# Kernel optimization log

Hardware: AMD Instinct MI355X
Metric: run time of the kernel (lower is better)

Reference implementation:

```python
import jax, jax.numpy as jnp
import numpy as np

N = 10000
E = 160000
H = 8
C = 128
D = 1024
NB = 3
NG = 64
NEG_SLOPE = 0.2
BN_EPS = 1e-5


def setup_inputs() -> dict:
    key = jax.random.key(0)
    ks = jax.random.split(key, 12)
    x = jax.random.normal(ks[0], (N, D), dtype=jnp.float32)
    edge_index = jax.random.randint(ks[1], (2, E), 0, N, dtype=jnp.int64)
    batch = jnp.sort(jax.random.randint(ks[2], (N,), 0, NG, dtype=jnp.int64))
    W = jax.random.normal(ks[3], (NB, D, D), dtype=jnp.float32) * 0.03
    att_src = jax.random.normal(ks[4], (NB, H, C), dtype=jnp.float32) * 0.1
    att_dst = jax.random.normal(ks[5], (NB, H, C), dtype=jnp.float32) * 0.1
    att_bias = jnp.zeros((NB, D), dtype=jnp.float32)
    gamma = jnp.ones((NB, D), dtype=jnp.float32)
    beta = jnp.zeros((NB, D), dtype=jnp.float32)
    W_out = jax.random.normal(ks[6], (D, 2), dtype=jnp.float32) * 0.03
    b_out = jnp.zeros((2,), dtype=jnp.float32)
    return {"x": x, "edge_index": edge_index, "batch": batch, "W": W,
            "att_src": att_src, "att_dst": att_dst, "att_bias": att_bias,
            "gamma": gamma, "beta": beta, "W_out": W_out, "b_out": b_out}


def _gat_conv(x, Wb, a_src, a_dst, bias, src, dst):
    # linear projection, per-head view: [N, H, C]
    h = (x @ Wb).reshape(N, H, C)
    alpha_src = jnp.einsum('nhc,hc->nh', h, a_src)  # [N,H]
    alpha_dst = jnp.einsum('nhc,hc->nh', h, a_dst)
    e = jax.nn.leaky_relu(alpha_src[src] + alpha_dst[dst], NEG_SLOPE)  # [Etot,H]
    # segment softmax over incoming edges per destination node
    m = jax.ops.segment_max(e, dst, num_segments=N)  # every node has self-loop
    ex = jnp.exp(e - m[dst])
    denom = jax.ops.segment_sum(ex, dst, num_segments=N)
    alpha = ex / denom[dst]  # [Etot,H]
    msg = alpha[:, :, None] * h[src]  # [Etot,H,C]
    out = jax.ops.segment_sum(msg, dst, num_segments=N).reshape(N, H * C)
    return out + bias


def _batchnorm(x, g, b):
    mu = jnp.mean(x, axis=0)
    var = jnp.mean(jnp.square(x - mu), axis=0)  # biased, training mode
    return (x - mu) * jax.lax.rsqrt(var + BN_EPS) * g + b


def reference(x, edge_index, batch, W, att_src, att_dst, att_bias, gamma, beta, W_out, b_out):
    # add self loops (PyG GATConv default)
    loop = jnp.arange(N, dtype=edge_index.dtype)
    src = jnp.concatenate([edge_index[0], loop])
    dst = jnp.concatenate([edge_index[1], loop])

    h = x
    prev = x
    for i in range(NB):
        att = _gat_conv(h, W[i], att_src[i], att_dst[i], att_bias[i], src, dst)
        o = jax.nn.relu(_batchnorm(prev + att, gamma[i], beta[i]))
        prev = h
        h = o

    # global mean pool over graphs
    sums = jax.ops.segment_sum(h, batch, num_segments=NG)
    cnts = jax.ops.segment_sum(jnp.ones((N,), dtype=h.dtype), batch, num_segments=NG)
    pooled = sums / jnp.maximum(cnts, 1.0)[:, None]
    return pooled @ W_out + b_out
```

## Files before the change

### kernel.cpp

```cpp
#include <hip/hip_runtime.h>
#include <hip/hip_bf16.h>

#define N_NODES 10000
#define E_EDGES 160000
#define ETOT    170000
#define H_HEADS 8
#define C_CH    128
#define D_DIM   1024
#define NBLK    3
#define NGRAPH  64
#define NEG_SLOPE 0.2f
#define BN_EPS  1e-5f

typedef __attribute__((ext_vector_type(8))) _Float16 half8;
typedef __attribute__((ext_vector_type(4))) _Float16 half4;
typedef __attribute__((ext_vector_type(2))) _Float16 half2v;
typedef __attribute__((ext_vector_type(4))) float f32x4;

__device__ inline int lower_bound_batch(const int* __restrict__ batch, int g) {
    int lo = 0, hi = N_NODES;
    while (lo < hi) {
        int mid = (lo + hi) >> 1;
        if (batch[mid] < g) lo = mid + 1;
        else hi = mid;
    }
    return lo;
}

__global__ void deg_kernel(const int* __restrict__ ei, int* __restrict__ deg) {
    int tid = blockIdx.x * blockDim.x + threadIdx.x;
    if (tid >= ETOT) return;
    int dst = (tid < E_EDGES) ? ei[E_EDGES + tid] : (tid - E_EDGES);
    atomicAdd(&deg[dst], 1);
}

__global__ void scan_kernel(const int* __restrict__ deg, int* __restrict__ ioff) {
    __shared__ int part[256];
    int t = threadIdx.x;
    const int CH = (N_NODES + 255) / 256;
    int base = t * CH;
    int s = 0;
    for (int j = 0; j < CH; ++j) {
        int idx = base + j;
        if (idx < N_NODES) s += deg[idx];
    }
    part[t] = s;
    __syncthreads();
    for (int o = 1; o < 256; o <<= 1) {
        int v = 0;
        if (t >= o) v = part[t - o];
        __syncthreads();
        part[t] += v;
        __syncthreads();
    }
    int run = (t == 0) ? 0 : part[t - 1];
    for (int j = 0; j < CH; ++j) {
        int idx = base + j;
        if (idx < N_NODES) { ioff[idx] = run; run += deg[idx]; }
    }
}

__global__ void scatter_kernel(const int* __restrict__ ei, int* __restrict__ ioff,
                               int* __restrict__ csr_src, int* __restrict__ csr_dst) {
    int tid = blockIdx.x * blockDim.x + threadIdx.x;
    if (tid >= ETOT) return;
    int src, dst;
    if (tid < E_EDGES) { src = ei[tid]; dst = ei[E_EDGES + tid]; }
    else { src = dst = tid - E_EDGES; }
    int pos = atomicAdd(&ioff[dst], 1);
    csr_src[pos] = src;
    csr_dst[pos] = dst;
}

__global__ __launch_bounds__(256) void xconv_kernel(const float* __restrict__ in,
                                                    _Float16* __restrict__ o, int n4) {
    int i = blockIdx.x * blockDim.x + threadIdx.x;
    if (i >= n4) return;
    float4 v = ((const float4*)in)[i];
    half4 h = {(_Float16)v.x, (_Float16)v.y, (_Float16)v.z, (_Float16)v.w};
    ((half4*)o)[i] = h;
}

__global__ __launch_bounds__(256) void wtconv_kernel(const float* __restrict__ Wall,
                                                     _Float16* __restrict__ t16all) {
    const float* W = Wall + (size_t)blockIdx.z * D_DIM * D_DIM;
    _Float16* t16 = t16all + (size_t)blockIdx.z * D_DIM * D_DIM;
    __shared__ float t[32][33];
    int bn = blockIdx.x * 32;
    int bk = blockIdx.y * 32;
    int tx = threadIdx.x & 31;
    int ty = threadIdx.x >> 5;
#pragma unroll
    for (int r = 0; r < 32; r += 8)
        t[ty + r][tx] = W[(size_t)(bk + ty + r) * D_DIM + bn + tx];
    __syncthreads();
#pragma unroll
    for (int r = 0; r < 32; r += 8)
        t16[(size_t)(bn + ty + r) * D_DIM + bk + tx] = (_Float16)t[tx][ty + r];
}

__global__ __launch_bounds__(256, 4) void gemm_mfma_kernel(const _Float16* __restrict__ A,
                                                           const _Float16* __restrict__ Bt,
                                                           _Float16* __restrict__ Hout,
                                                           const float* __restrict__ att_s,
                                                           const float* __restrict__ att_d,
                                                           float* __restrict__ asrc,
                                                           float* __restrict__ adst,
                                                           float* __restrict__ stats, int M) {
    __shared__ short As[128 * 64];
    __shared__ short Bs[64 * 64];
    int bx = blockIdx.x;
    int tid = threadIdx.x;
    if (bx == 0) {
#pragma unroll
        for (int j = 0; j < 8; ++j) stats[tid + j * 256] = 0.f;
    }
    int c = bx & 7;
    int nt = (bx >> 3) & 15;
    int mt = c + 8 * (bx >> 7);
    if (mt >= 79) return;
    int bm = mt * 128;
    int head = nt >> 1;
    int bncol = (nt & 1) * 64;
    int bnrow = nt * 64;
    int wave = tid >> 6;
    int lane = tid & 63;
    int wm = wave * 32;
    int quad = lane >> 4;
    int l16 = lane & 15;

    f32x4 acc[2][4];
#pragma unroll
    for (int i = 0; i < 2; ++i)
#pragma unroll
        for (int j = 0; j < 4; ++j) acc[i][j] = (f32x4){0.f, 0.f, 0.f, 0.f};

    int srow8 = lane >> 3;
    int sswz = ((lane & 7) ^ srow8) << 4;
    const char* gA[4];
    const char* gB[2];
    char* ldA[4];
    char* ldB[2];
#pragma unroll
    for (int r = 0; r < 4; ++r) {
        int arow = wave * 8 + r * 32 + srow8;
        int ga = bm + arow;
        if (ga > M - 1) ga = M - 1;
        gA[r] = (const char*)(A + (size_t)ga * 1024) + sswz;
        ldA[r] = (char*)As + (wave * 8 + r * 32) * 128;
    }
#pragma unroll
    for (int r = 0; r < 2; ++r) {
        int brow = wave * 8 + r * 32 + srow8;
        gB[r] = (const char*)(Bt + (size_t)(bnrow + brow) * 1024) + sswz;
        ldB[r] = (char*)Bs + (wave * 8 + r * 32) * 128;
    }

    int xr = l16 & 7;
    for (int kb = 0; kb < 16; ++kb) {
        int ko = kb * 128;
#pragma unroll
        for (int r = 0; r < 4; ++r)
            __builtin_amdgcn_global_load_lds(
                (const __attribute__((address_space(1))) void*)(gA[r] + ko),
                (__attribute__((address_space(3))) void*)ldA[r], 16, 0, 0);
#pragma unroll
        for (int r = 0; r < 2; ++r)
            __builtin_amdgcn_global_load_lds(
                (const __attribute__((address_space(1))) void*)(gB[r] + ko),
                (__attribute__((address_space(3))) void*)ldB[r], 16, 0, 0);
        __syncthreads();
#pragma unroll
        for (int h = 0; h < 2; ++h) {
            int sl = (quad + h * 4) ^ xr;
            half8 af[2], bfr[4];
#pragma unroll
            for (int i = 0; i < 2; ++i)
                af[i] = *(const half8*)(As + (wm + i * 16 + l16) * 64 + sl * 8);
#pragma unroll
            for (int j = 0; j < 4; ++j)
                bfr[j] = *(const half8*)(Bs + (j * 16 + l16) * 64 + sl * 8);
#pragma unroll
            for (int i = 0; i < 2; ++i)
#pragma unroll
                for (int j = 0; j < 4; ++j)
                    acc[i][j] = __builtin_amdgcn_mfma_f32_16x16x32_f16(af[i], bfr[j], acc[i][j], 0, 0, 0);
        }
        __syncthreads();
    }

    float wsv[4], wdv[4];
#pragma unroll
    for (int j = 0; j < 4; ++j) {
        int cc = bncol + j * 16 + l16;
        wsv[j] = att_s[head * 128 + cc];
        wdv[j] = att_d[head * 128 + cc];
    }
#pragma unroll
    for (int i = 0; i < 2; ++i) {
#pragma unroll
        for (int reg = 0; reg < 4; ++reg) {
            float p = acc[i][0][reg] * wsv[0] + acc[i][1][reg] * wsv[1] +
                      acc[i][2][reg] * wsv[2] + acc[i][3][reg] * wsv[3];
            float q = acc[i][0][reg] * wdv[0] + acc[i][1][reg] * wdv[1] +
                      acc[i][2][reg] * wdv[2] + acc[i][3][reg] * wdv[3];
#pragma unroll
            for (int o = 1; o < 16; o <<= 1) {
                p += __shfl_xor(p, o);
                q += __shfl_xor(q, o);
            }
            if (l16 == 0) {
                int gr = bm + wm + i * 16 + quad * 4 + reg;
                if (gr < M) {
                    atomicAdd(&asrc[gr * 8 + head], p);
                    atomicAdd(&adst[gr * 8 + head], q);
                }
            }
        }
    }
#pragma unroll
    for (int i = 0; i < 2; ++i) {
#pragma unroll
        for (int reg = 0; reg < 4; ++reg) {
            int gr = bm + wm + i * 16 + quad * 4 + reg;
            if (gr < M) {
                _Float16* hp = Hout + (size_t)head * N_NODES * 128 + (size_t)gr * 128 + bncol + l16;
#pragma unroll
                for (int j = 0; j < 4; ++j) hp[j * 16] = (_Float16)acc[i][j][reg];
            }
        }
    }
}

__global__ __launch_bounds__(256) void edge_exp_kernel(const int* __restrict__ csr_src,
                                                       const int* __restrict__ csr_dst,
                                                       const float* __restrict__ asrc,
                                                       const float* __restrict__ adst,
                                                       float* __restrict__ exw) {
    int p = blockIdx.x * 256 + threadIdx.x;
    if (p >= ETOT) return;
    int s = csr_src[p];
    int d = csr_dst[p];
    float4 s0 = *(const float4*)(asrc + (unsigned)s * 8u);
    float4 s1 = *(const float4*)(asrc + (unsigned)s * 8u + 4u);
    float4 d0 = *(const float4*)(adst + (unsigned)d * 8u);
    float4 d1 = *(const float4*)(adst + (unsigned)d * 8u + 4u);
    float e[8] = {s0.x + d0.x, s0.y + d0.y, s0.z + d0.z, s0.w + d0.w,
                  s1.x + d1.x, s1.y + d1.y, s1.z + d1.z, s1.w + d1.w};
#pragma unroll
    for (int j = 0; j < 8; ++j) {
        float v = e[j];
        v = (v > 0.f) ? v : NEG_SLOPE * v;
        exw[j * ETOT + p] = __expf(v);
    }
}

__global__ __launch_bounds__(256) void agg_kernel(const _Float16* __restrict__ h16,
                                                  const float* __restrict__ exw,
                                                  const int* __restrict__ ioff,
                                                  const int* __restrict__ csr_src,
                                                  const _Float16* __restrict__ prevh,
                                                  const float* __restrict__ bias,
                                                  _Float16* __restrict__ yout) {
    int bx = blockIdx.x;
    int head = bx & 7;
    int wave = threadIdx.x >> 6;
    int lane = threadIdx.x & 63;
    int sub = lane >> 4;
    int l16 = lane & 15;
    unsigned c8 = (unsigned)(l16 * 8);
    int n = (bx >> 3) * 4 + wave;
    const _Float16* hh = h16 + (size_t)head * N_NODES * 128;
    const float* exh = exw + (size_t)head * ETOT;
    int start = (n == 0) ? 0 : ioff[n - 1];
    int end = ioff[n];
    float den = 0.f;
    float acc[8];
#pragma unroll
    for (int j = 0; j < 8; ++j) acc[j] = 0.f;
    int p = start;
    for (; p + 8 <= end; p += 8) {
        int sA = csr_src[p + sub];
        int sB = csr_src[p + 4 + sub];
        float xA = exh[p + sub];
        float xB = exh[p + 4 + sub];
        half8 hA = *(const half8*)(hh + ((unsigned)sA * 128u + c8));
        half8 hB = *(const half8*)(hh + ((unsigned)sB * 128u + c8));
        den += xA + xB;
#pragma unroll
        for (int j = 0; j < 8; ++j)
            acc[j] = fmaf(xA, (float)hA[j], fmaf(xB, (float)hB[j], acc[j]));
    }
    for (; p + 4 <= end; p += 4) {
        int s = csr_src[p + sub];
        float x = exh[p + sub];
        half8 hv = *(const half8*)(hh + ((unsigned)s * 128u + c8));
        den += x;
#pragma unroll
        for (int j = 0; j < 8; ++j)
            acc[j] = fmaf(x, (float)hv[j], acc[j]);
    }
    if (p + sub < end) {
        int s = csr_src[p + sub];
        float x = exh[p + sub];
        half8 hv = *(const half8*)(hh + ((unsigned)s * 128u + c8));
        den += x;
#pragma unroll
        for (int j = 0; j < 8; ++j)
            acc[j] = fmaf(x, (float)hv[j], acc[j]);
    }
#pragma unroll
    for (int j = 0; j < 8; ++j) {
        acc[j] += __shfl_xor(acc[j], 16);
        acc[j] += __shfl_xor(acc[j], 32);
    }
    den += __shfl_xor(den, 16);
    den += __shfl_xor(den, 32);
    if (sub == 0) {
        float invd = 1.0f / den;
        int col = head * 128 + l16 * 8;
        half8 ph = *(const half8*)(prevh + (size_t)n * 1024 + col);
        float4 b0 = *(const float4*)(bias + col);
        float4 b1 = *(const float4*)(bias + col + 4);
        half8 o;
        o[0] = (_Float16)fmaf(acc[0], invd, (float)ph[0] + b0.x);
        o[1] = (_Float16)fmaf(acc[1], invd, (float)ph[1] + b0.y);
        o[2] = (_Float16)fmaf(acc[2], invd, (float)ph[2] + b0.z);
        o[3] = (_Float16)fmaf(acc[3], invd, (float)ph[3] + b0.w);
        o[4] = (_Float16)fmaf(acc[4], invd, (float)ph[4] + b1.x);
        o[5] = (_Float16)fmaf(acc[5], invd, (float)ph[5] + b1.y);
        o[6] = (_Float16)fmaf(acc[6], invd, (float)ph[6] + b1.z);
        o[7] = (_Float16)fmaf(acc[7], invd, (float)ph[7] + b1.w);
        *(half8*)(yout + (size_t)n * 1024 + col) = o;
    }
}

__global__ void bn_stats_kernel(const _Float16* __restrict__ y, float* __restrict__ stats) {
    int col = (blockIdx.x * 256 + threadIdx.x) * 2;
    float s0 = 0.f, s1 = 0.f, q0 = 0.f, q1 = 0.f;
    for (int r = blockIdx.y; r < N_NODES; r += gridDim.y) {
        half2v v = *(const half2v*)(y + (size_t)r * 1024 + col);
        float a = (float)v[0], b = (float)v[1];
        s0 += a; q0 += a * a;
        s1 += b; q1 += b * b;
    }
    atomicAdd(&stats[col], s0);
    atomicAdd(&stats[col + 1], s1);
    atomicAdd(&stats[1024 + col], q0);
    atomicAdd(&stats[1024 + col + 1], q1);
}

__global__ void bn_apply_kernel(const _Float16* __restrict__ y, const float* __restrict__ stats,
                                const float* __restrict__ gamma, const float* __restrict__ beta,
                                _Float16* __restrict__ oout, float* __restrict__ azero) {
    int idx4 = blockIdx.x * blockDim.x + threadIdx.x;
    if (idx4 < 2 * N_NODES * H_HEADS / 4)
        ((float4*)azero)[idx4] = make_float4(0.f, 0.f, 0.f, 0.f);
    if (idx4 >= N_NODES * D_DIM / 4) return;
    int base = idx4 * 4;
    int col = base & 1023;
    const float invN = 1.0f / (float)N_NODES;
    half4 v = ((const half4*)y)[idx4];
    float r[4];
#pragma unroll
    for (int j = 0; j < 4; ++j) {
        int cc = col + j;
        float mu = stats[cc] * invN;
        float var = stats[1024 + cc] * invN - mu * mu;
        float t = ((float)v[j] - mu) * rsqrtf(var + BN_EPS) * gamma[cc] + beta[cc];
        r[j] = fmaxf(t, 0.f);
    }
    half4 h = {(_Float16)r[0], (_Float16)r[1], (_Float16)r[2], (_Float16)r[3]};
    ((half4*)oout)[idx4] = h;
}

__global__ __launch_bounds__(256) void pool_kernel(const _Float16* __restrict__ h3,
                                                   const int* __restrict__ batch,
                                                   float* __restrict__ pooled) {
    int g = blockIdx.y;
    int col = threadIdx.x * 4;
    int lo = lower_bound_batch(batch, g);
    int hi = lower_bound_batch(batch, g + 1);
    int len = hi - lo;
    int r0 = lo + (int)(((long long)len * blockIdx.x) >> 3);
    int r1 = lo + (int)(((long long)len * (blockIdx.x + 1)) >> 3);
    float a0 = 0.f, a1 = 0.f, a2 = 0.f, a3 = 0.f;
    for (int r = r0; r < r1; ++r) {
        half4 v = *(const half4*)(h3 + (size_t)r * 1024 + col);
        a0 += (float)v[0]; a1 += (float)v[1]; a2 += (float)v[2]; a3 += (float)v[3];
    }
    if (r1 > r0) {
        atomicAdd(&pooled[(size_t)g * 1024 + col + 0], a0);
        atomicAdd(&pooled[(size_t)g * 1024 + col + 1], a1);
        atomicAdd(&pooled[(size_t)g * 1024 + col + 2], a2);
        atomicAdd(&pooled[(size_t)g * 1024 + col + 3], a3);
    }
}

__global__ void final_kernel(const float* __restrict__ pooled, const int* __restrict__ batch,
                             const float* __restrict__ Wout, const float* __restrict__ bout,
                             float* __restrict__ out) {
    int g = blockIdx.x;
    int t = threadIdx.x;
    float p0 = 0.f, p1 = 0.f;
    for (int d = t; d < 1024; d += 256) {
        float v = pooled[(size_t)g * 1024 + d];
        p0 = fmaf(v, Wout[2 * d], p0);
        p1 = fmaf(v, Wout[2 * d + 1], p1);
    }
    __shared__ float s0[256], s1[256];
    s0[t] = p0; s1[t] = p1;
    __syncthreads();
    for (int o = 128; o; o >>= 1) {
        if (t < o) { s0[t] += s0[t + o]; s1[t] += s1[t + o]; }
        __syncthreads();
    }
    if (t == 0) {
        int cnt = lower_bound_batch(batch, g + 1) - lower_bound_batch(batch, g);
        float inv = 1.0f / fmaxf((float)cnt, 1.0f);
        out[g * 2 + 0] = s0[0] * inv + bout[0];
        out[g * 2 + 1] = s1[0] * inv + bout[1];
    }
}

extern "C" void kernel_launch(void* const* d_in, const int* in_sizes, int n_in,
                              void* d_out, int out_size, void* d_ws, size_t ws_size,
                              hipStream_t stream) {
    const float* x        = (const float*)d_in[0];
    const int*   ei       = (const int*)d_in[1];
    const int*   batch    = (const int*)d_in[2];
    const float* W        = (const float*)d_in[3];
    const float* att_src  = (const float*)d_in[4];
    const float* att_dst  = (const float*)d_in[5];
    const float* att_bias = (const float*)d_in[6];
    const float* gamma    = (const float*)d_in[7];
    const float* beta     = (const float*)d_in[8];
    const float* Wout     = (const float*)d_in[9];
    const float* bout     = (const float*)d_in[10];
    float* out = (float*)d_out;

    const size_t ND = (size_t)N_NODES * D_DIM;
    float* ws = (float*)d_ws;
    float* asrc   = ws;
    float* adst   = asrc + (size_t)N_NODES * H_HEADS;
    float* stats  = adst + (size_t)N_NODES * H_HEADS;
    float* pooled = stats + 2 * D_DIM;
    int* ideg     = (int*)(pooled + (size_t)NGRAPH * D_DIM);
    int* ioff     = ideg + N_NODES;
    int* csr_src  = ioff + N_NODES;
    int* csr_dst  = csr_src + ETOT;
    float* exw    = (float*)(csr_dst + ETOT);
    _Float16* bufP  = (_Float16*)(exw + (size_t)ETOT * H_HEADS);
    _Float16* bufO0 = bufP + ND;
    _Float16* h16   = bufO0 + ND;
    _Float16* y16   = h16 + ND;
    _Float16* Wt3   = y16 + ND;

    hipMemsetAsync(ideg, 0, N_NODES * sizeof(int), stream);
    hipMemsetAsync(pooled, 0, (size_t)NGRAPH * D_DIM * sizeof(float), stream);
    hipMemsetAsync(asrc, 0, (size_t)2 * N_NODES * H_HEADS * sizeof(float), stream);
    deg_kernel<<<(ETOT + 255) / 256, 256, 0, stream>>>(ei, ideg);
    scan_kernel<<<1, 256, 0, stream>>>(ideg, ioff);
    scatter_kernel<<<(ETOT + 255) / 256, 256, 0, stream>>>(ei, ioff, csr_src, csr_dst);
    xconv_kernel<<<(int)(ND / 4 + 255) / 256, 256, 0, stream>>>(x, bufP, (int)(ND / 4));
    wtconv_kernel<<<dim3(32, 32, 3), 256, 0, stream>>>(W, Wt3);

    const _Float16* Ain[3]  = {bufP, bufO0, bufP};
    const _Float16* Pin[3]  = {bufP, bufP, bufO0};
    _Float16* Oout[3]       = {bufO0, bufP, bufP};

    for (int i = 0; i < NBLK; ++i) {
        gemm_mfma_kernel<<<1280, 256, 0, stream>>>(
            Ain[i], Wt3 + (size_t)i * D_DIM * D_DIM, h16,
            att_src + i * H_HEADS * C_CH, att_dst + i * H_HEADS * C_CH,
            asrc, adst, stats, N_NODES);
        edge_exp_kernel<<<(ETOT + 255) / 256, 256, 0, stream>>>(csr_src, csr_dst,
                                                                asrc, adst, exw);
        agg_kernel<<<(N_NODES / 4) * H_HEADS, 256, 0, stream>>>(
            h16, exw, ioff, csr_src, Pin[i], att_bias + i * D_DIM, y16);
        bn_stats_kernel<<<dim3(2, 128), 256, 0, stream>>>(y16, stats);
        bn_apply_kernel<<<(int)(ND / 4 + 255) / 256, 256, 0, stream>>>(
            y16, stats, gamma + i * D_DIM, beta + i * D_DIM, Oout[i], asrc);
    }

    pool_kernel<<<dim3(8, NGRAPH), 256, 0, stream>>>(bufP, batch, pooled);
    final_kernel<<<NGRAPH, 256, 0, stream>>>(pooled, batch, Wout, bout, out);
}
```

Before: 545.6 us.

## Double-buffer LDS tiles in MFMA GEMM to overlap global loads with compute

The projection GEMM now keeps two LDS buffers for the A and B tiles. It issues the async global-to-LDS loads for the next K-step before computing on the current one, and the loop is unrolled by two to ping-pong between the buffers. The goal is to hide global memory latency behind MFMA work instead of stalling at each barrier. LDS use per block doubles to 48KB, which may reduce occupancy under the launch bounds of 4 blocks per CU.

```diff
diff --git a/kernel.cpp b/kernel.cpp
--- a/kernel.cpp
+++ b/kernel.cpp
@@ -107,8 +107,8 @@
                                                            float* __restrict__ asrc,
                                                            float* __restrict__ adst,
                                                            float* __restrict__ stats, int M) {
-    __shared__ short As[128 * 64];
-    __shared__ short Bs[64 * 64];
+    __shared__ short As[2 * 128 * 64];
+    __shared__ short Bs[2 * 64 * 64];
     int bx = blockIdx.x;
     int tid = threadIdx.x;
     if (bx == 0) {
@@ -139,55 +139,76 @@
     int sswz = ((lane & 7) ^ srow8) << 4;
     const char* gA[4];
     const char* gB[2];
-    char* ldA[4];
-    char* ldB[2];
+    char* ldA0[4];
+    char* ldA1[4];
+    char* ldB0[2];
+    char* ldB1[2];
 #pragma unroll
     for (int r = 0; r < 4; ++r) {
         int arow = wave * 8 + r * 32 + srow8;
         int ga = bm + arow;
         if (ga > M - 1) ga = M - 1;
         gA[r] = (const char*)(A + (size_t)ga * 1024) + sswz;
-        ldA[r] = (char*)As + (wave * 8 + r * 32) * 128;
+        ldA0[r] = (char*)As + (wave * 8 + r * 32) * 128;
+        ldA1[r] = ldA0[r] + 16384;
     }
 #pragma unroll
     for (int r = 0; r < 2; ++r) {
         int brow = wave * 8 + r * 32 + srow8;
         gB[r] = (const char*)(Bt + (size_t)(bnrow + brow) * 1024) + sswz;
-        ldB[r] = (char*)Bs + (wave * 8 + r * 32) * 128;
-    }
+        ldB0[r] = (char*)Bs + (wave * 8 + r * 32) * 128;
+        ldB1[r] = ldB0[r] + 8192;
+    }
+
+#define STAGE(LA, LB, kbyte)                                                          \
+    do {                                                                              \
+        _Pragma("unroll")                                                             \
+        for (int r = 0; r < 4; ++r)                                                   \
+            __builtin_amdgcn_global_load_lds(                                         \
+                (const __attribute__((address_space(1))) void*)(gA[r] + (kbyte)),     \
+                (__attribute__((address_space(3))) void*)(LA)[r], 16, 0, 0);          \
+        _Pragma("unroll")                                                             \
+        for (int r = 0; r < 2; ++r)                                                   \
+            __builtin_amdgcn_global_load_lds(                                         \
+                (const __attribute__((address_space(1))) void*)(gB[r] + (kbyte)),     \
+                (__attribute__((address_space(3))) void*)(LB)[r], 16, 0, 0);          \
+    } while (0)
+
+#define COMPUTE(Ab, Bb)                                                               \
+    do {                                                                              \
+        _Pragma("unroll")                                                             \
+        for (int h = 0; h < 2; ++h) {                                                 \
+            int sl = (quad + h * 4) ^ xr;                                             \
+            half8 af[2], bfr[4];                                                      \
+            _Pragma("unroll")                                                         \
+            for (int i = 0; i < 2; ++i)                                               \
+                af[i] = *(const half8*)((Ab) + (wm + i * 16 + l16) * 64 + sl * 8);    \
+            _Pragma("unroll")                                                         \
+            for (int j = 0; j < 4; ++j)                                               \
+                bfr[j] = *(const half8*)((Bb) + (j * 16 + l16) * 64 + sl * 8);        \
+            _Pragma("unroll")                                                         \
+            for (int i = 0; i < 2; ++i)                                               \
+                _Pragma("unroll")                                                     \
+                for (int j = 0; j < 4; ++j)                                           \
+                    acc[i][j] = __builtin_amdgcn_mfma_f32_16x16x32_f16(af[i], bfr[j], acc[i][j], 0, 0, 0); \
+        }                                                                             \
+    } while (0)
 
     int xr = l16 & 7;
-    for (int kb = 0; kb < 16; ++kb) {
-        int ko = kb * 128;
-#pragma unroll
-        for (int r = 0; r < 4; ++r)
-            __builtin_amdgcn_global_load_lds(
-                (const __attribute__((address_space(1))) void*)(gA[r] + ko),
-                (__attribute__((address_space(3))) void*)ldA[r], 16, 0, 0);
-#pragma unroll
-        for (int r = 0; r < 2; ++r)
-            __builtin_amdgcn_global_load_lds(
-                (const __attribute__((address_space(1))) void*)(gB[r] + ko),
-                (__attribute__((address_space(3))) void*)ldB[r], 16, 0, 0);
+    STAGE(ldA0, ldB0, 0);
+    __syncthreads();
+    for (int kb2 = 0; kb2 < 8; ++kb2) {
+        int kA = kb2 * 2;
+        STAGE(ldA1, ldB1, (kA + 1) * 128);
+        COMPUTE(As, Bs);
         __syncthreads();
-#pragma unroll
-        for (int h = 0; h < 2; ++h) {
-            int sl = (quad + h * 4) ^ xr;
-            half8 af[2], bfr[4];
-#pragma unroll
-            for (int i = 0; i < 2; ++i)
-                af[i] = *(const half8*)(As + (wm + i * 16 + l16) * 64 + sl * 8);
-#pragma unroll
-            for (int j = 0; j < 4; ++j)
-                bfr[j] = *(const half8*)(Bs + (j * 16 + l16) * 64 + sl * 8);
-#pragma unroll
-            for (int i = 0; i < 2; ++i)
-#pragma unroll
-                for (int j = 0; j < 4; ++j)
-                    acc[i][j] = __builtin_amdgcn_mfma_f32_16x16x32_f16(af[i], bfr[j], acc[i][j], 0, 0, 0);
-        }
+        if (kb2 < 7)
+            STAGE(ldA0, ldB0, (kA + 2) * 128);
+        COMPUTE(As + 8192, Bs + 4096);
         __syncthreads();
     }
+#undef STAGE
+#undef COMPUTE
 
     float wsv[4], wdv[4];
 #pragma unroll
```

Result: slower. 579.7 us (+6.2%).
